# Kernel tuning notes

Hardware: AMD Instinct MI355X
Metric: run time of the kernel (lower is better)

Reference implementation:

```python
import jax, jax.numpy as jnp
import numpy as np

N_NODES = 100000
N_EDGES = 400000
F_IN = 128
HID = 128
HEADS = 4
N_GRAPHS = 2000
NEG_SLOPE = 0.2  # GATConv leaky relu slope
BN_EPS = 1e-5


def setup_inputs() -> dict:
    key = jax.random.key(0)
    ks = jax.random.split(key, 20)
    s = 0.05
    d = {}
    d["x"] = jax.random.normal(ks[0], (N_NODES, F_IN), jnp.float32)
    d["edge_index"] = jax.random.randint(ks[1], (2, N_EDGES), 0, N_NODES, jnp.int32)
    d["batch"] = jnp.sort(jax.random.randint(ks[2], (N_NODES,), 0, N_GRAPHS, jnp.int32))
    # GCN stack (first layer in=F_IN==HID so stackable)
    d["gcn_W"] = jax.random.normal(ks[3], (3, HID, HID), jnp.float32) * s
    d["gcn_b"] = jax.random.normal(ks[4], (3, HID), jnp.float32) * s
    # BatchNorm (eval mode: running stats)
    d["bn_gamma"] = jnp.ones((3, HID), jnp.float32)
    d["bn_beta"] = jnp.zeros((3, HID), jnp.float32)
    d["bn_mean"] = jax.random.normal(ks[5], (3, HID), jnp.float32) * s
    d["bn_var"] = jax.random.uniform(ks[6], (3, HID), jnp.float32, 0.5, 1.5)
    # GAT (heads=4, concat=False -> mean over heads)
    d["gat_W"] = jax.random.normal(ks[7], (HID, HEADS * HID), jnp.float32) * s
    d["gat_att_src"] = jax.random.normal(ks[8], (HEADS, HID), jnp.float32) * s
    d["gat_att_dst"] = jax.random.normal(ks[9], (HEADS, HID), jnp.float32) * s
    d["gat_b"] = jax.random.normal(ks[10], (HID,), jnp.float32) * s
    # classifier 128 -> 64 -> 32 -> 1
    d["c1_W"] = jax.random.normal(ks[11], (HID, HID // 2), jnp.float32) * s
    d["c1_b"] = jnp.zeros((HID // 2,), jnp.float32)
    d["c2_W"] = jax.random.normal(ks[12], (HID // 2, HID // 4), jnp.float32) * s
    d["c2_b"] = jnp.zeros((HID // 4,), jnp.float32)
    d["c3_W"] = jax.random.normal(ks[13], (HID // 4, 1), jnp.float32) * s
    d["c3_b"] = jnp.zeros((1,), jnp.float32)
    return d


def reference(x, edge_index, batch, gcn_W, gcn_b, bn_gamma, bn_beta, bn_mean, bn_var,
              gat_W, gat_att_src, gat_att_dst, gat_b,
              c1_W, c1_b, c2_W, c2_b, c3_W, c3_b):
    N = x.shape[0]
    loops = jnp.arange(N, dtype=edge_index.dtype)
    src = jnp.concatenate([edge_index[0], loops])  # messages flow src -> dst
    dst = jnp.concatenate([edge_index[1], loops])

    # GCN symmetric normalization with self loops
    deg = jax.ops.segment_sum(jnp.ones_like(dst, jnp.float32), dst, N)
    dinv = jnp.where(deg > 0, jax.lax.rsqrt(deg), 0.0)
    enorm = (dinv[src] * dinv[dst])[:, None]  # [E+N, 1]

    h = x
    for i in range(3):
        t = h @ gcn_W[i]                                   # [N, HID]
        agg = jax.ops.segment_sum(t[src] * enorm, dst, N) + gcn_b[i]
        agg = (agg - bn_mean[i]) * jax.lax.rsqrt(bn_var[i] + BN_EPS) * bn_gamma[i] + bn_beta[i]
        agg = jax.nn.relu(agg)
        h = h + agg if i > 0 else agg                      # residual from layer 1

    # GAT, heads=4, concat=False (mean over heads), with self loops
    hh = (h @ gat_W).reshape(N, HEADS, HID)
    a_s = jnp.einsum('nhd,hd->nh', hh, gat_att_src)
    a_d = jnp.einsum('nhd,hd->nh', hh, gat_att_dst)
    e = jax.nn.leaky_relu(a_s[src] + a_d[dst], NEG_SLOPE)  # [E+N, HEADS]
    emax = jax.ops.segment_max(e, dst, N)                  # every node has a self loop
    ex = jnp.exp(e - emax[dst])
    denom = jax.ops.segment_sum(ex, dst, N)
    alpha = ex / (denom[dst] + 1e-16)
    att = jax.ops.segment_sum(hh[src] * alpha[:, :, None], dst, N)  # [N, HEADS, HID]
    h = h + (att.mean(axis=1) + gat_b)

    # global mean pool over graphs
    gsum = jax.ops.segment_sum(h, batch, N_GRAPHS)
    cnt = jax.ops.segment_sum(jnp.ones((N, 1), jnp.float32), batch, N_GRAPHS)
    g = gsum / jnp.maximum(cnt, 1.0)

    z = jax.nn.relu(g @ c1_W + c1_b)
    z = jax.nn.relu(z @ c2_W + c2_b)
    return z @ c3_W + c3_b  # [N_GRAPHS, 1]
```

## Files before the change

kernel.cpp:

```cpp
#include <hip/hip_runtime.h>
#include <math.h>

#define NN 100000
#define NE 400000
#define HID 128
#define HEADS 4
#define NG 2000
#define BN_EPS 1e-5f
#define NEG_SLOPE 0.2f
#define NB_SCAN 391

__global__ void k_zero_i(int* __restrict__ p, int n) {
    int i = blockIdx.x * blockDim.x + threadIdx.x;
    if (i < n) p[i] = 0;
}

__global__ void k_count(const int* __restrict__ dst, int* __restrict__ cnt) {
    int e = blockIdx.x * blockDim.x + threadIdx.x;
    if (e < NE) atomicAdd(&cnt[dst[e]], 1);
}

__global__ void k_dinv2(const int* __restrict__ cnt, float* __restrict__ dinv) {
    int n = blockIdx.x * blockDim.x + threadIdx.x;
    if (n < NN) dinv[n] = rsqrtf((float)cnt[n] + 1.0f);
}

__global__ __launch_bounds__(256) void k_bsum(const int* __restrict__ cnt, int* __restrict__ bsum) {
    __shared__ int s[256];
    int tid = threadIdx.x;
    int n = blockIdx.x * 256 + tid;
    s[tid] = (n < NN) ? cnt[n] : 0;
    __syncthreads();
    for (int off = 128; off > 0; off >>= 1) {
        if (tid < off) s[tid] += s[tid + off];
        __syncthreads();
    }
    if (tid == 0) bsum[blockIdx.x] = s[0];
}

__global__ __launch_bounds__(512) void k_bscan(int* __restrict__ bsum, int* __restrict__ row_ptr) {
    __shared__ int s[512];
    int tid = threadIdx.x;
    int v = (tid < NB_SCAN) ? bsum[tid] : 0;
    s[tid] = v;
    __syncthreads();
    for (int off = 1; off < 512; off <<= 1) {
        int t_ = (tid >= off) ? s[tid - off] : 0;
        __syncthreads();
        s[tid] += t_;
        __syncthreads();
    }
    if (tid < NB_SCAN) bsum[tid] = s[tid] - v;
    if (tid == 0) row_ptr[NN] = NE;
}

__global__ __launch_bounds__(256) void k_rowptr(const int* __restrict__ cnt, const int* __restrict__ boff,
                                                int* __restrict__ row_ptr) {
    __shared__ int s[256];
    int tid = threadIdx.x;
    int n = blockIdx.x * 256 + tid;
    int v = (n < NN) ? cnt[n] : 0;
    s[tid] = v;
    __syncthreads();
    for (int off = 1; off < 256; off <<= 1) {
        int t_ = (tid >= off) ? s[tid - off] : 0;
        __syncthreads();
        s[tid] += t_;
        __syncthreads();
    }
    if (n < NN) row_ptr[n] = boff[blockIdx.x] + s[tid] - v;
}

__global__ void k_csr(const int* __restrict__ src, const int* __restrict__ dst,
                      const int* __restrict__ row_ptr, int* __restrict__ fill,
                      const float* __restrict__ dinv,
                      int* __restrict__ csr_src, float* __restrict__ csr_w) {
    int e = blockIdx.x * blockDim.x + threadIdx.x;
    if (e >= NE) return;
    int s = src[e], d = dst[e];
    int pos = row_ptr[d] + atomicAdd(&fill[d], 1);
    csr_src[pos] = s;
    csr_w[pos] = dinv[s] * dinv[d];
}

__global__ __launch_bounds__(512) void k_gemm128(const float* __restrict__ A,
                                                 const float* __restrict__ W,
                                                 float* __restrict__ C,
                                                 int nrows, int ldw, int coffW,
                                                 const float* __restrict__ att_s,
                                                 const float* __restrict__ att_d,
                                                 float* __restrict__ as_out,
                                                 float* __restrict__ ad_out) {
    __shared__ float Ws[64][128];
    __shared__ float As[128][64];
    int tid = threadIdx.x;
    int row0 = blockIdx.x * 128;
    int c0 = (tid & 31) * 4;
    int r0 = (tid >> 5) * 8;
    float acc[8][4] = {};
    for (int kb = 0; kb < 2; ++kb) {
        __syncthreads();
        for (int i = tid; i < 2048; i += 512) {
            int k  = i >> 5;
            int c4 = (i & 31) * 4;
            *(float4*)&Ws[k][c4] =
                *(const float4*)&W[(long)(kb * 64 + k) * ldw + coffW + c4];
        }
        for (int i = tid; i < 2048; i += 512) {
            int r  = i >> 4;
            int k4 = (i & 15) * 4;
            int gr = row0 + r;
            float4 v = (gr < nrows)
                ? *(const float4*)&A[(long)gr * 128 + kb * 64 + k4]
                : make_float4(0.f, 0.f, 0.f, 0.f);
            *(float4*)&As[r][k4] = v;
        }
        __syncthreads();
        for (int k4 = 0; k4 < 64; k4 += 4) {
            float4 a4[8];
#pragma unroll
            for (int j = 0; j < 8; ++j) a4[j] = *(const float4*)&As[r0 + j][k4];
#pragma unroll
            for (int i = 0; i < 4; ++i) {
                float4 wv = *(const float4*)&Ws[k4 + i][c0];
#pragma unroll
                for (int j = 0; j < 8; ++j) {
                    float a = (i == 0) ? a4[j].x : (i == 1) ? a4[j].y : (i == 2) ? a4[j].z : a4[j].w;
                    acc[j][0] += a * wv.x;
                    acc[j][1] += a * wv.y;
                    acc[j][2] += a * wv.z;
                    acc[j][3] += a * wv.w;
                }
            }
        }
    }
#pragma unroll
    for (int j = 0; j < 8; ++j) {
        int gr = row0 + r0 + j;
        if (gr < nrows)
            *(float4*)&C[(long)gr * 128 + c0] =
                make_float4(acc[j][0], acc[j][1], acc[j][2], acc[j][3]);
    }
    if (att_s) {
#pragma unroll
        for (int j = 0; j < 8; ++j) {
            float ps = acc[j][0] * att_s[c0] + acc[j][1] * att_s[c0 + 1]
                     + acc[j][2] * att_s[c0 + 2] + acc[j][3] * att_s[c0 + 3];
            float pd = acc[j][0] * att_d[c0] + acc[j][1] * att_d[c0 + 1]
                     + acc[j][2] * att_d[c0 + 2] + acc[j][3] * att_d[c0 + 3];
#pragma unroll
            for (int off = 16; off > 0; off >>= 1) {
                ps += __shfl_down(ps, off, 32);
                pd += __shfl_down(pd, off, 32);
            }
            int gr = row0 + r0 + j;
            if ((tid & 31) == 0 && gr < nrows) { as_out[gr] = ps; ad_out[gr] = pd; }
        }
    }
}

__global__ __launch_bounds__(128) void k_gcn_agg(const float* __restrict__ t,
                                                 const int* __restrict__ row_ptr,
                                                 const int* __restrict__ csr_src,
                                                 const float* __restrict__ csr_w,
                                                 const float* __restrict__ dinv,
                                                 const float* __restrict__ b,
                                                 const float* __restrict__ gamma,
                                                 const float* __restrict__ beta,
                                                 const float* __restrict__ mean,
                                                 const float* __restrict__ var,
                                                 float* __restrict__ h, int residual) {
    int n = blockIdx.x;
    int d = threadIdx.x;
    int e0 = row_ptr[n], e1 = row_ptr[n + 1];
    float dn = dinv[n];
    float acc = t[(long)n * HID + d] * dn * dn;
    for (int j = e0; j < e1; ++j)
        acc += t[(long)csr_src[j] * HID + d] * csr_w[j];
    float v = acc + b[d];
    v = (v - mean[d]) * rsqrtf(var[d] + BN_EPS) * gamma[d] + beta[d];
    v = fmaxf(v, 0.f);
    long idx = (long)n * HID + d;
    h[idx] = residual ? (h[idx] + v) : v;
}

__global__ __launch_bounds__(128) void k_gat_agg(const float* __restrict__ t,
                                                 const int* __restrict__ row_ptr,
                                                 const int* __restrict__ csr_src,
                                                 const float* __restrict__ a_s,
                                                 const float* __restrict__ a_d,
                                                 const float* __restrict__ gat_b,
                                                 float* __restrict__ agg,
                                                 float* __restrict__ h, int mode) {
    int n = blockIdx.x;
    int d = threadIdx.x;
    int e0 = row_ptr[n], e1 = row_ptr[n + 1];
    float adn = a_d[n];
    float es = a_s[n] + adn;
    es = (es > 0.f) ? es : NEG_SLOPE * es;
    float m = es;
    for (int j = e0; j < e1; ++j) {
        float e = a_s[csr_src[j]] + adn;
        e = (e > 0.f) ? e : NEG_SLOPE * e;
        m = fmaxf(m, e);
    }
    float w0 = expf(es - m);
    float denom = w0;
    float acc = t[(long)n * HID + d] * w0;
    for (int j = e0; j < e1; ++j) {
        int s = csr_src[j];
        float e = a_s[s] + adn;
        e = (e > 0.f) ? e : NEG_SLOPE * e;
        float w = expf(e - m);
        denom += w;
        acc += t[(long)s * HID + d] * w;
    }
    acc = 0.25f * acc / (denom + 1e-16f);
    long idx = (long)n * HID + d;
    if (mode == 0)      agg[idx] = acc;
    else if (mode == 1) agg[idx] += acc;
    else                h[idx] += agg[idx] + acc + gat_b[d];
}

__global__ __launch_bounds__(128) void k_pool_cls(const float* __restrict__ h,
                                                  const int* __restrict__ batch,
                                                  const float* __restrict__ c1W,
                                                  const float* __restrict__ c1b,
                                                  const float* __restrict__ c2W,
                                                  const float* __restrict__ c2b,
                                                  const float* __restrict__ c3W,
                                                  const float* __restrict__ c3b,
                                                  float* __restrict__ out) {
    int g = blockIdx.x;
    int tid = threadIdx.x;
    int lo = 0, hb = NN;
    while (lo < hb) { int mid = (lo + hb) >> 1; if (batch[mid] < g) lo = mid + 1; else hb = mid; }
    int a = lo, b2 = NN;
    while (a < b2) { int mid = (a + b2) >> 1; if (batch[mid] < g + 1) a = mid + 1; else b2 = mid; }
    int hi = a;
    float s = 0.f;
    for (int n = lo; n < hi; ++n) s += h[(long)n * HID + tid];
    __shared__ float gbuf[HID];
    __shared__ float z1buf[64];
    __shared__ float z2buf[32];
    gbuf[tid] = s / fmaxf((float)(hi - lo), 1.f);
    __syncthreads();
    if (tid < 64) {
        float acc = c1b[tid];
        for (int d2 = 0; d2 < 128; ++d2) acc += gbuf[d2] * c1W[d2 * 64 + tid];
        z1buf[tid] = fmaxf(acc, 0.f);
    }
    __syncthreads();
    if (tid < 32) {
        float acc = c2b[tid];
        for (int d2 = 0; d2 < 64; ++d2) acc += z1buf[d2] * c2W[d2 * 32 + tid];
        z2buf[tid] = fmaxf(acc, 0.f);
    }
    __syncthreads();
    if (tid < 32) {
        float p = z2buf[tid] * c3W[tid];
#pragma unroll
        for (int off = 16; off > 0; off >>= 1) p += __shfl_down(p, off, 32);
        if (tid == 0) out[g] = p + c3b[0];
    }
}

extern "C" void kernel_launch(void* const* d_in, const int* in_sizes, int n_in,
                              void* d_out, int out_size, void* d_ws, size_t ws_size,
                              hipStream_t stream) {
    const float* x     = (const float*)d_in[0];
    const int*   ei    = (const int*)d_in[1];
    const int*   src   = ei;
    const int*   dst   = ei + NE;
    const int*   batch = (const int*)d_in[2];
    const float* gcn_W = (const float*)d_in[3];
    const float* gcn_b = (const float*)d_in[4];
    const float* bn_g  = (const float*)d_in[5];
    const float* bn_be = (const float*)d_in[6];
    const float* bn_m  = (const float*)d_in[7];
    const float* bn_v  = (const float*)d_in[8];
    const float* gat_W = (const float*)d_in[9];
    const float* att_s = (const float*)d_in[10];
    const float* att_d = (const float*)d_in[11];
    const float* gat_b = (const float*)d_in[12];
    const float* c1W = (const float*)d_in[13];
    const float* c1b = (const float*)d_in[14];
    const float* c2W = (const float*)d_in[15];
    const float* c2b = (const float*)d_in[16];
    const float* c3W = (const float*)d_in[17];
    const float* c3b = (const float*)d_in[18];
    float* out = (float*)d_out;

    float* ws = (float*)d_ws;
    size_t o = 0;
    float* dinv    = ws + o; o += NN;
    int*   cnt     = (int*)(ws + o); o += NN;
    int*   bsum    = (int*)(ws + o); o += 512;
    int*   row_ptr = (int*)(ws + o); o += NN + 1;
    int*   csr_src = (int*)(ws + o); o += NE;
    float* csr_w   = ws + o; o += NE;
    float* h       = ws + o; o += (size_t)NN * HID;
    float* t       = ws + o; o += (size_t)NN * HID;
    float* agg     = ws + o; o += (size_t)NN * HID;
    float* a_s     = ws + o; o += NN;
    float* a_d     = ws + o; o += NN;

    auto cdiv = [](long a, long b) { return (int)((a + b - 1) / b); };

    k_zero_i<<<cdiv(NN, 256), 256, 0, stream>>>(cnt, NN);
    k_count<<<cdiv(NE, 256), 256, 0, stream>>>(dst, cnt);
    k_dinv2<<<cdiv(NN, 256), 256, 0, stream>>>(cnt, dinv);
    k_bsum<<<NB_SCAN, 256, 0, stream>>>(cnt, bsum);
    k_bscan<<<1, 512, 0, stream>>>(bsum, row_ptr);
    k_rowptr<<<NB_SCAN, 256, 0, stream>>>(cnt, bsum, row_ptr);
    k_zero_i<<<cdiv(NN, 256), 256, 0, stream>>>(cnt, NN);
    k_csr<<<cdiv(NE, 256), 256, 0, stream>>>(src, dst, row_ptr, cnt, dinv, csr_src, csr_w);

    const float* hin = x;
    for (int L = 0; L < 3; ++L) {
        k_gemm128<<<cdiv(NN, 128), 512, 0, stream>>>(hin, gcn_W + (size_t)L * HID * HID, t,
                                                     NN, HID, 0, nullptr, nullptr, nullptr, nullptr);
        k_gcn_agg<<<NN, 128, 0, stream>>>(t, row_ptr, csr_src, csr_w, dinv,
                                          gcn_b + L * HID, bn_g + L * HID, bn_be + L * HID,
                                          bn_m + L * HID, bn_v + L * HID, h, L > 0);
        hin = h;
    }

    for (int hd = 0; hd < HEADS; ++hd) {
        k_gemm128<<<cdiv(NN, 128), 512, 0, stream>>>(h, gat_W, t, NN, HEADS * HID, hd * HID,
                                                     att_s + hd * HID, att_d + hd * HID, a_s, a_d);
        k_gat_agg<<<NN, 128, 0, stream>>>(t, row_ptr, csr_src, a_s, a_d, gat_b, agg, h,
                                          hd == 0 ? 0 : (hd == HEADS - 1 ? 2 : 1));
    }

    k_pool_cls<<<NG, 128, 0, stream>>>(h, batch, c1W, c1b, c2W, c2b, c3W, c3b, out);
}
```

Before: 1.347 ms.

## Vectorize GCN/GAT aggregation with float4 and precompute GAT attention weights

The GCN and GAT aggregation kernels now handle four nodes per 128-thread block, with each 32-lane group loading float4 feature slices rather than each thread handling one float. GAT softmax weights are now computed once per node and head in a separate per-node kernel that stores normalized alpha per edge and a self weight. Before, every one of the 128 threads per node redid the max and exp passes. This removes redundant exp work and widens memory accesses. The cost is an extra kernel launch per head and an alpha array that is written and then read back.

```diff
diff --git a/kernel.cpp b/kernel.cpp
--- a/kernel.cpp
+++ b/kernel.cpp
@@ -170,30 +170,43 @@
                                                  const float* __restrict__ mean,
                                                  const float* __restrict__ var,
                                                  float* __restrict__ h, int residual) {
-    int n = blockIdx.x;
-    int d = threadIdx.x;
-    int e0 = row_ptr[n], e1 = row_ptr[n + 1];
-    float dn = dinv[n];
-    float acc = t[(long)n * HID + d] * dn * dn;
-    for (int j = e0; j < e1; ++j)
-        acc += t[(long)csr_src[j] * HID + d] * csr_w[j];
-    float v = acc + b[d];
-    v = (v - mean[d]) * rsqrtf(var[d] + BN_EPS) * gamma[d] + beta[d];
-    v = fmaxf(v, 0.f);
-    long idx = (long)n * HID + d;
-    h[idx] = residual ? (h[idx] + v) : v;
-}
-
-__global__ __launch_bounds__(128) void k_gat_agg(const float* __restrict__ t,
-                                                 const int* __restrict__ row_ptr,
-                                                 const int* __restrict__ csr_src,
-                                                 const float* __restrict__ a_s,
-                                                 const float* __restrict__ a_d,
-                                                 const float* __restrict__ gat_b,
-                                                 float* __restrict__ agg,
-                                                 float* __restrict__ h, int mode) {
-    int n = blockIdx.x;
-    int d = threadIdx.x;
+    int node = blockIdx.x * 4 + (threadIdx.x >> 5);
+    if (node >= NN) return;
+    int c = (threadIdx.x & 31) * 4;
+    int e0 = row_ptr[node], e1 = row_ptr[node + 1];
+    float dn = dinv[node];
+    float sw = dn * dn;
+    float4 acc = *(const float4*)&t[(long)node * HID + c];
+    acc.x *= sw; acc.y *= sw; acc.z *= sw; acc.w *= sw;
+    for (int j = e0; j < e1; ++j) {
+        int s = csr_src[j];
+        float w = csr_w[j];
+        float4 v = *(const float4*)&t[(long)s * HID + c];
+        acc.x += v.x * w; acc.y += v.y * w; acc.z += v.z * w; acc.w += v.w * w;
+    }
+    float4 bb = *(const float4*)&b[c];
+    float4 mm = *(const float4*)&mean[c];
+    float4 vv = *(const float4*)&var[c];
+    float4 gg = *(const float4*)&gamma[c];
+    float4 be = *(const float4*)&beta[c];
+    float4 r;
+    r.x = fmaxf((acc.x + bb.x - mm.x) * rsqrtf(vv.x + BN_EPS) * gg.x + be.x, 0.f);
+    r.y = fmaxf((acc.y + bb.y - mm.y) * rsqrtf(vv.y + BN_EPS) * gg.y + be.y, 0.f);
+    r.z = fmaxf((acc.z + bb.z - mm.z) * rsqrtf(vv.z + BN_EPS) * gg.z + be.z, 0.f);
+    r.w = fmaxf((acc.w + bb.w - mm.w) * rsqrtf(vv.w + BN_EPS) * gg.w + be.w, 0.f);
+    long idx = (long)node * HID + c;
+    if (residual) {
+        float4 hp = *(const float4*)&h[idx];
+        r.x += hp.x; r.y += hp.y; r.z += hp.z; r.w += hp.w;
+    }
+    *(float4*)&h[idx] = r;
+}
+
+__global__ void k_gat_w(const int* __restrict__ row_ptr, const int* __restrict__ csr_src,
+                        const float* __restrict__ a_s, const float* __restrict__ a_d,
+                        float* __restrict__ alpha, float* __restrict__ selfw) {
+    int n = blockIdx.x * blockDim.x + threadIdx.x;
+    if (n >= NN) return;
     int e0 = row_ptr[n], e1 = row_ptr[n + 1];
     float adn = a_d[n];
     float es = a_s[n] + adn;
@@ -206,20 +219,57 @@
     }
     float w0 = expf(es - m);
     float denom = w0;
-    float acc = t[(long)n * HID + d] * w0;
+    for (int j = e0; j < e1; ++j) {
+        float e = a_s[csr_src[j]] + adn;
+        e = (e > 0.f) ? e : NEG_SLOPE * e;
+        float w = expf(e - m);
+        alpha[j] = w;
+        denom += w;
+    }
+    float inv = 1.f / (denom + 1e-16f);
+    selfw[n] = w0 * inv;
+    for (int j = e0; j < e1; ++j) alpha[j] *= inv;
+}
+
+__global__ __launch_bounds__(128) void k_gat_agg(const float* __restrict__ t,
+                                                 const int* __restrict__ row_ptr,
+                                                 const int* __restrict__ csr_src,
+                                                 const float* __restrict__ alpha,
+                                                 const float* __restrict__ selfw,
+                                                 const float* __restrict__ gat_b,
+                                                 float* __restrict__ agg,
+                                                 float* __restrict__ h, int mode) {
+    int node = blockIdx.x * 4 + (threadIdx.x >> 5);
+    if (node >= NN) return;
+    int c = (threadIdx.x & 31) * 4;
+    int e0 = row_ptr[node], e1 = row_ptr[node + 1];
+    float sw = selfw[node];
+    float4 acc = *(const float4*)&t[(long)node * HID + c];
+    acc.x *= sw; acc.y *= sw; acc.z *= sw; acc.w *= sw;
     for (int j = e0; j < e1; ++j) {
         int s = csr_src[j];
-        float e = a_s[s] + adn;
-        e = (e > 0.f) ? e : NEG_SLOPE * e;
-        float w = expf(e - m);
-        denom += w;
-        acc += t[(long)s * HID + d] * w;
-    }
-    acc = 0.25f * acc / (denom + 1e-16f);
-    long idx = (long)n * HID + d;
-    if (mode == 0)      agg[idx] = acc;
-    else if (mode == 1) agg[idx] += acc;
-    else                h[idx] += agg[idx] + acc + gat_b[d];
+        float w = alpha[j];
+        float4 v = *(const float4*)&t[(long)s * HID + c];
+        acc.x += v.x * w; acc.y += v.y * w; acc.z += v.z * w; acc.w += v.w * w;
+    }
+    acc.x *= 0.25f; acc.y *= 0.25f; acc.z *= 0.25f; acc.w *= 0.25f;
+    long idx = (long)node * HID + c;
+    if (mode == 0) {
+        *(float4*)&agg[idx] = acc;
+    } else if (mode == 1) {
+        float4 p = *(const float4*)&agg[idx];
+        p.x += acc.x; p.y += acc.y; p.z += acc.z; p.w += acc.w;
+        *(float4*)&agg[idx] = p;
+    } else {
+        float4 p = *(const float4*)&agg[idx];
+        float4 hp = *(const float4*)&h[idx];
+        float4 gb = *(const float4*)&gat_b[c];
+        hp.x += p.x + acc.x + gb.x;
+        hp.y += p.y + acc.y + gb.y;
+        hp.z += p.z + acc.z + gb.z;
+        hp.w += p.w + acc.w + gb.w;
+        *(float4*)&h[idx] = hp;
+    }
 }
 
 __global__ __launch_bounds__(128) void k_pool_cls(const float* __restrict__ h,
@@ -296,7 +346,7 @@
     float* dinv    = ws + o; o += NN;
     int*   cnt     = (int*)(ws + o); o += NN;
     int*   bsum    = (int*)(ws + o); o += 512;
-    int*   row_ptr = (int*)(ws + o); o += NN + 1;
+    int*   row_ptr = (int*)(ws + o); o += NN + 4;
     int*   csr_src = (int*)(ws + o); o += NE;
     float* csr_w   = ws + o; o += NE;
     float* h       = ws + o; o += (size_t)NN * HID;
@@ -304,6 +354,8 @@
     float* agg     = ws + o; o += (size_t)NN * HID;
     float* a_s     = ws + o; o += NN;
     float* a_d     = ws + o; o += NN;
+    float* alpha   = ws + o; o += NE;
+    float* selfw   = ws + o; o += NN;
 
     auto cdiv = [](long a, long b) { return (int)((a + b - 1) / b); };
 
@@ -320,7 +372,7 @@
     for (int L = 0; L < 3; ++L) {
         k_gemm128<<<cdiv(NN, 128), 512, 0, stream>>>(hin, gcn_W + (size_t)L * HID * HID, t,
                                                      NN, HID, 0, nullptr, nullptr, nullptr, nullptr);
-        k_gcn_agg<<<NN, 128, 0, stream>>>(t, row_ptr, csr_src, csr_w, dinv,
+        k_gcn_agg<<<cdiv(NN, 4), 128, 0, stream>>>(t, row_ptr, csr_src, csr_w, dinv,
                                           gcn_b + L * HID, bn_g + L * HID, bn_be + L * HID,
                                           bn_m + L * HID, bn_v + L * HID, h, L > 0);
         hin = h;
@@ -329,7 +381,8 @@
     for (int hd = 0; hd < HEADS; ++hd) {
         k_gemm128<<<cdiv(NN, 128), 512, 0, stream>>>(h, gat_W, t, NN, HEADS * HID, hd * HID,
                                                      att_s + hd * HID, att_d + hd * HID, a_s, a_d);
-        k_gat_agg<<<NN, 128, 0, stream>>>(t, row_ptr, csr_src, a_s, a_d, gat_b, agg, h,
+        k_gat_w<<<cdiv(NN, 256), 256, 0, stream>>>(row_ptr, csr_src, a_s, a_d, alpha, selfw);
+        k_gat_agg<<<cdiv(NN, 4), 128, 0, stream>>>(t, row_ptr, csr_src, alpha, selfw, gat_b, agg, h,
                                           hd == 0 ? 0 : (hd == HEADS - 1 ? 2 : 1));
     }
 
```

Measured after the change: 1.151 ms. 14.6% less time.
